# Optimization experiments

Measured on AMD Instinct MI355X. Metric: run time of the kernel, lower is better.

Reference implementation:

```python
import jax, jax.numpy as jnp
import numpy as np

B, T, D_IN, D_OUT = 4, 2048, 1024, 1024


def setup_inputs() -> dict:
    key = jax.random.key(0)
    k1, k2, k3, k4 = jax.random.split(key, 4)
    s = 0.02  # keep activations in a sane range
    x = jax.random.normal(k1, (B, T, D_IN), dtype=jnp.float32)
    Wq = jax.random.normal(k2, (D_IN, D_OUT), dtype=jnp.float32) * s
    Wk = jax.random.normal(k3, (D_IN, D_OUT), dtype=jnp.float32) * s
    Wv = jax.random.normal(k4, (D_IN, D_OUT), dtype=jnp.float32) * s
    return {"x": x, "Wq": Wq, "Wk": Wk, "Wv": Wv}


def reference(x, Wq, Wk, Wv):
    # Linear projections (torch Linear: y = x @ W^T, here W stored as [d_in, d_out])
    q = jnp.einsum('btd,de->bte', x, Wq)
    k = jnp.einsum('btd,de,->bte', x, Wk, jnp.float32(1.0)) if False else jnp.einsum('btd,de->bte', x, Wk)
    v = jnp.einsum('btd,de->bte', x, Wv)
    # Full [B, T, T] score matrix (faithful to the hand-rolled implementation)
    scores = jnp.einsum('bqe,bke->bqk', q, k)
    T_ = x.shape[1]
    causal = jnp.triu(jnp.ones((T_, T_), dtype=bool), k=1)  # True above diagonal
    scores = jnp.where(causal[None, :, :], -jnp.inf, scores)
    scale = 1.0 / jnp.sqrt(jnp.asarray(k.shape[-1], dtype=scores.dtype))
    attn = jax.nn.softmax(scores * scale, axis=-1)
    # dropout p=0.0 -> identity
    return jnp.einsum('bqk,bke->bqe', attn, v)
```

## Files before the change

### kernel.cpp

```cpp
#include <hip/hip_runtime.h>
#include <hip/hip_bf16.h>
#include <cstdint>

typedef __attribute__((ext_vector_type(8))) short short8;
typedef __attribute__((ext_vector_type(4))) float floatx4;

__device__ __forceinline__ float bf2f(unsigned short u) {
  unsigned int x = ((unsigned int)u) << 16;
  return __builtin_bit_cast(float, x);
}
__device__ __forceinline__ unsigned short f2bf(float f) {
  unsigned int x = __builtin_bit_cast(unsigned int, f);
  x += 0x7fffu + ((x >> 16) & 1u);
  return (unsigned short)(x >> 16);
}

__device__ __forceinline__ void gload_lds16(const void* g, void* l) {
  __builtin_amdgcn_global_load_lds(
      (const __attribute__((address_space(1))) void*)g,
      (__attribute__((address_space(3))) void*)l, 16, 0, 0);
}


__global__ __launch_bounds__(256) void cvtx_kernel(const float* __restrict__ x,
                                                   unsigned short* __restrict__ xb) {
  int i = blockIdx.x * 256 + threadIdx.x;
  const float4* xf = (const float4*)x;
  float4 a = xf[i * 2], b = xf[i * 2 + 1];
  short8 o;
  o[0] = (short)f2bf(a.x); o[1] = (short)f2bf(a.y);
  o[2] = (short)f2bf(a.z); o[3] = (short)f2bf(a.w);
  o[4] = (short)f2bf(b.x); o[5] = (short)f2bf(b.y);
  o[6] = (short)f2bf(b.z); o[7] = (short)f2bf(b.w);
  ((short8*)xb)[i] = o;
}

__global__ __launch_bounds__(256) void wt_kernel(const float* __restrict__ Wq,
                                                 const float* __restrict__ Wk,
                                                 const float* __restrict__ Wv,
                                                 unsigned short* __restrict__ Wt) {
  int z = blockIdx.z;
  const float* W = z == 0 ? Wq : (z == 1 ? Wk : Wv);
  unsigned short* O = Wt + (size_t)z * 1024 * 1024;
  __shared__ float tile[64][65];
  int c0 = blockIdx.x * 64;
  int r0 = blockIdx.y * 64;
  int tid = threadIdx.x;
#pragma unroll
  for (int i = 0; i < 4; ++i) {
    int c = tid + i * 256; int rr = c >> 4, q = c & 15;
    float4 v = *(const float4*)&W[(size_t)(r0 + rr) * 1024 + c0 + q * 4];
    tile[rr][q * 4 + 0] = v.x; tile[rr][q * 4 + 1] = v.y;
    tile[rr][q * 4 + 2] = v.z; tile[rr][q * 4 + 3] = v.w;
  }
  __syncthreads();
#pragma unroll
  for (int i = 0; i < 2; ++i) {
    int c = tid + i * 256; int oc = c >> 3, q = c & 7;
    short8 o;
#pragma unroll
    for (int j = 0; j < 8; ++j) o[j] = (short)f2bf(tile[q * 8 + j][oc]);
    *(short8*)&O[(size_t)(c0 + oc) * 1024 + r0 + q * 8] = o;
  }
}

__global__ __launch_bounds__(256) void vt_kernel(const unsigned short* __restrict__ V,
                                                 unsigned short* __restrict__ Vt) {
  int b = blockIdx.z;
  const unsigned short* Vb = V + (size_t)b * 2048 * 1024;
  unsigned short* Vtb = Vt + (size_t)b * 1024 * 2048;
  __shared__ unsigned short tile[64][72];
  int t0 = blockIdx.x * 64;
  int e0 = blockIdx.y * 64;
  int tid = threadIdx.x;
#pragma unroll
  for (int i = 0; i < 2; ++i) {
    int c = tid + i * 256; int rr = c >> 3, q = c & 7;
    short8 s = *(const short8*)&Vb[(size_t)(t0 + rr) * 1024 + e0 + q * 8];
#pragma unroll
    for (int j = 0; j < 8; ++j) tile[rr][q * 8 + j] = (unsigned short)s[j];
  }
  __syncthreads();
#pragma unroll
  for (int i = 0; i < 2; ++i) {
    int c = tid + i * 256; int er = c >> 3, q = c & 7;
    short8 o;
#pragma unroll
    for (int j = 0; j < 8; ++j) o[j] = (short)tile[q * 8 + j][er];
    *(short8*)&Vtb[(size_t)(e0 + er) * 2048 + t0 + q * 8] = o;
  }
}


template <bool OUT_BF16>
__device__ __forceinline__ void gemm_tn_core(const unsigned short* __restrict__ A,
                                             const unsigned short* __restrict__ B,
                                             void* __restrict__ C,
                                             int lda, int ldb, int ldc,
                                             int m0, int n0, int kTiles) {
  __shared__ __align__(16) unsigned short Asm[2][128 * 32];
  __shared__ __align__(16) unsigned short Bsm[2][128 * 32];
  const int tid = threadIdx.x;
  const int lane = tid & 63;
  const int wave = tid >> 6;
  const int wrow = (wave >> 1) * 64;
  const int wcol = (wave & 1) * 64;
  const int r15 = lane & 15;
  const int kg = (lane >> 4) * 8;

  floatx4 acc[4][4] = {};

  const unsigned short* Ag = A + (size_t)m0 * lda;
  const unsigned short* Bg = B + (size_t)n0 * ldb;

  auto stage = [&](int buf, int kt) {
    int k0 = kt * 32;
#pragma unroll
    for (int i = 0; i < 2; ++i) {
      int c = tid + i * 256;
      gload_lds16(Ag + (size_t)(c >> 2) * lda + k0 + (c & 3) * 8, &Asm[buf][c * 8]);
    }
#pragma unroll
    for (int i = 0; i < 2; ++i) {
      int c = tid + i * 256;
      gload_lds16(Bg + (size_t)(c >> 2) * ldb + k0 + (c & 3) * 8, &Bsm[buf][c * 8]);
    }
  };

  stage(0, 0);
  for (int kt = 0; kt < kTiles; ++kt) {
    int cur = kt & 1;
    __syncthreads();
    if (kt + 1 < kTiles) stage(cur ^ 1, kt + 1);
    const unsigned short* As = Asm[cur];
    const unsigned short* Bs = Bsm[cur];
    short8 af[4], bfr[4];
#pragma unroll
    for (int m = 0; m < 4; ++m)
      af[m] = *(const short8*)&As[(wrow + m * 16 + r15) * 32 + kg];
#pragma unroll
    for (int n = 0; n < 4; ++n)
      bfr[n] = *(const short8*)&Bs[(wcol + n * 16 + r15) * 32 + kg];
#pragma unroll
    for (int m = 0; m < 4; ++m)
#pragma unroll
      for (int n = 0; n < 4; ++n)
        acc[m][n] = __builtin_amdgcn_mfma_f32_16x16x32_bf16(af[m], bfr[n], acc[m][n], 0, 0, 0);
  }

  const int rq = (lane >> 4) * 4;
#pragma unroll
  for (int m = 0; m < 4; ++m) {
#pragma unroll
    for (int n = 0; n < 4; ++n) {
      int gc = n0 + wcol + n * 16 + r15;
#pragma unroll
      for (int r = 0; r < 4; ++r) {
        int gr = m0 + wrow + m * 16 + rq + r;
        if (OUT_BF16)
          ((unsigned short*)C)[(size_t)gr * ldc + gc] = f2bf(acc[m][n][r]);
        else
          ((float*)C)[(size_t)gr * ldc + gc] = acc[m][n][r];
      }
    }
  }
}

__global__ __launch_bounds__(256) void qkv_kernel(const unsigned short* __restrict__ Xb,
                                                  const unsigned short* __restrict__ Wt,
                                                  unsigned short* __restrict__ QKV) {
  gemm_tn_core<true>(Xb, Wt + (size_t)blockIdx.z * 1024 * 1024,
                     QKV + (size_t)blockIdx.z * 8192 * 1024,
                     1024, 1024, 1024, blockIdx.x * 128, blockIdx.y * 128, 32);
}

__global__ __launch_bounds__(256) void s_kernel(const unsigned short* __restrict__ Q,
                                                const unsigned short* __restrict__ K,
                                                unsigned short* __restrict__ S) {
  int t = blockIdx.x;
  int qb = (int)((sqrtf(8.f * (float)t + 1.f) - 1.f) * 0.5f);
  while ((qb + 1) * (qb + 2) / 2 <= t) ++qb;
  while (qb * (qb + 1) / 2 > t) --qb;
  int kb = t - qb * (qb + 1) / 2;
  size_t b = blockIdx.y;
  gemm_tn_core<true>(Q + b * 2048 * 1024, K + b * 2048 * 1024, S + b * 2048 * 2048,
                     1024, 1024, 2048, qb * 128, kb * 128, 32);
}

__global__ __launch_bounds__(256) void pv_kernel(const unsigned short* __restrict__ P,
                                                 const unsigned short* __restrict__ Vt,
                                                 float* __restrict__ O) {
  int qb = blockIdx.x;
  size_t b = blockIdx.z;
  gemm_tn_core<false>(P + b * 2048 * 2048, Vt + b * 1024 * 2048, O + b * 2048 * 1024,
                      2048, 2048, 1024, qb * 128, blockIdx.y * 128, (qb + 1) * 4);
}

__global__ __launch_bounds__(256) void softmax_kernel(unsigned short* __restrict__ S) {
  const int r = blockIdx.x;
  const int b = blockIdx.y;
  unsigned short* row = S + ((size_t)b * 2048 + r) * 2048;
  const int len = r + 1;
  const int padEnd = ((r >> 7) + 1) << 7;
  const int tid = threadIdx.x;
  const int base = tid * 8;
  const float scale = 0.03125f;

  float v[8];
  float mymax = -1e30f;
  if (base < len) {
    short8 s = *(const short8*)(row + base);
#pragma unroll
    for (int j = 0; j < 8; ++j) {
      float f = (base + j < len) ? bf2f((unsigned short)s[j]) : -1e30f;
      v[j] = f;
      mymax = fmaxf(mymax, f);
    }
  } else {
#pragma unroll
    for (int j = 0; j < 8; ++j) v[j] = -1e30f;
  }

  __shared__ float redm[4], reds[4];
  const int wave = tid >> 6, lane = tid & 63;
#pragma unroll
  for (int off = 32; off > 0; off >>= 1) mymax = fmaxf(mymax, __shfl_xor(mymax, off, 64));
  if (lane == 0) redm[wave] = mymax;
  __syncthreads();
  float m = fmaxf(fmaxf(redm[0], redm[1]), fmaxf(redm[2], redm[3])) * scale;

  float p[8];
  float mysum = 0.f;
#pragma unroll
  for (int j = 0; j < 8; ++j) {
    float e = (base + j < len) ? __expf(v[j] * scale - m) : 0.f;
    p[j] = e;
    mysum += e;
  }
#pragma unroll
  for (int off = 32; off > 0; off >>= 1) mysum += __shfl_xor(mysum, off, 64);
  if (lane == 0) reds[wave] = mysum;
  __syncthreads();
  float inv = 1.f / (reds[0] + reds[1] + reds[2] + reds[3]);

  if (base < padEnd) {
    short8 o;
#pragma unroll
    for (int j = 0; j < 8; ++j) o[j] = (short)f2bf(p[j] * inv);
    *(short8*)(row + base) = o;
  }
}


extern "C" void kernel_launch(void* const* d_in, const int* in_sizes, int n_in,
                              void* d_out, int out_size, void* d_ws, size_t ws_size,
                              hipStream_t stream) {
  const float* x  = (const float*)d_in[0];
  const float* Wq = (const float*)d_in[1];
  const float* Wk = (const float*)d_in[2];
  const float* Wv = (const float*)d_in[3];
  float* out = (float*)d_out;

  unsigned short* Xb  = (unsigned short*)d_ws;
  unsigned short* Wt  = Xb + (size_t)8192 * 1024;
  unsigned short* QKV = Wt + (size_t)3 * 1024 * 1024;
  unsigned short* Vt  = QKV + (size_t)3 * 8192 * 1024;
  unsigned short* S   = Vt + (size_t)4 * 1024 * 2048;

  const unsigned short* Qp = QKV;
  const unsigned short* Kp = QKV + (size_t)8192 * 1024;
  const unsigned short* Vp = QKV + (size_t)2 * 8192 * 1024;

  hipLaunchKernelGGL(cvtx_kernel, dim3(4096), dim3(256), 0, stream, x, Xb);
  hipLaunchKernelGGL(wt_kernel, dim3(16, 16, 3), dim3(256), 0, stream, Wq, Wk, Wv, Wt);
  hipLaunchKernelGGL(qkv_kernel, dim3(64, 8, 3), dim3(256), 0, stream, Xb, Wt, QKV);
  hipLaunchKernelGGL(vt_kernel, dim3(32, 16, 4), dim3(256), 0, stream, Vp, Vt);
  hipLaunchKernelGGL(s_kernel, dim3(136, 4), dim3(256), 0, stream, Qp, Kp, S);
  hipLaunchKernelGGL(softmax_kernel, dim3(2048, 4), dim3(256), 0, stream, S);
  hipLaunchKernelGGL(pv_kernel, dim3(16, 8, 4), dim3(256), 0, stream, S, Vt, out);
}
```

Before: 194.1 us.

## Replace QKV projection GEMM with 256x256 8-wave pipelined swizzled kernel

Replaces the 128x128 four-wave QKV projection GEMM with an eight-wave kernel using 256x256 output tiles over the fused 3072-wide weight matrix. It adds XOR-swizzled LDS layouts to avoid bank conflicts, a deeper multi-stage global-to-LDS prefetch with explicit vmcnt waits and barriers, MFMA priority boosting, and workgroup index swizzling for L2 locality. The goal is more data reuse per tile and better overlap of loads with MFMA work in the largest GEMM. The larger accumulator footprint raises register pressure, and the hand-placed waitcnt and barrier logic is fragile.

```diff
diff --git a/kernel.cpp b/kernel.cpp
--- a/kernel.cpp
+++ b/kernel.cpp
@@ -4,15 +4,16 @@
 
 typedef __attribute__((ext_vector_type(8))) short short8;
 typedef __attribute__((ext_vector_type(4))) float floatx4;
-
-__device__ __forceinline__ float bf2f(unsigned short u) {
+typedef unsigned short ushort;
+
+__device__ __forceinline__ float bf2f(ushort u) {
   unsigned int x = ((unsigned int)u) << 16;
   return __builtin_bit_cast(float, x);
 }
-__device__ __forceinline__ unsigned short f2bf(float f) {
+__device__ __forceinline__ ushort f2bf(float f) {
   unsigned int x = __builtin_bit_cast(unsigned int, f);
   x += 0x7fffu + ((x >> 16) & 1u);
-  return (unsigned short)(x >> 16);
+  return (ushort)(x >> 16);
 }
 
 __device__ __forceinline__ void gload_lds16(const void* g, void* l) {
@@ -23,7 +24,7 @@
 
 
 __global__ __launch_bounds__(256) void cvtx_kernel(const float* __restrict__ x,
-                                                   unsigned short* __restrict__ xb) {
+                                                   ushort* __restrict__ xb) {
   int i = blockIdx.x * 256 + threadIdx.x;
   const float4* xf = (const float4*)x;
   float4 a = xf[i * 2], b = xf[i * 2 + 1];
@@ -38,10 +39,10 @@
 __global__ __launch_bounds__(256) void wt_kernel(const float* __restrict__ Wq,
                                                  const float* __restrict__ Wk,
                                                  const float* __restrict__ Wv,
-                                                 unsigned short* __restrict__ Wt) {
+                                                 ushort* __restrict__ Wt) {
   int z = blockIdx.z;
   const float* W = z == 0 ? Wq : (z == 1 ? Wk : Wv);
-  unsigned short* O = Wt + (size_t)z * 1024 * 1024;
+  ushort* O = Wt + (size_t)z * 1024 * 1024;
   __shared__ float tile[64][65];
   int c0 = blockIdx.x * 64;
   int r0 = blockIdx.y * 64;
@@ -64,12 +65,12 @@
   }
 }
 
-__global__ __launch_bounds__(256) void vt_kernel(const unsigned short* __restrict__ V,
-                                                 unsigned short* __restrict__ Vt) {
+__global__ __launch_bounds__(256) void vt_kernel(const ushort* __restrict__ V,
+                                                 ushort* __restrict__ Vt) {
   int b = blockIdx.z;
-  const unsigned short* Vb = V + (size_t)b * 2048 * 1024;
-  unsigned short* Vtb = Vt + (size_t)b * 1024 * 2048;
-  __shared__ unsigned short tile[64][72];
+  const ushort* Vb = V + (size_t)b * 2048 * 1024;
+  ushort* Vtb = Vt + (size_t)b * 1024 * 2048;
+  __shared__ ushort tile[64][72];
   int t0 = blockIdx.x * 64;
   int e0 = blockIdx.y * 64;
   int tid = threadIdx.x;
@@ -78,7 +79,7 @@
     int c = tid + i * 256; int rr = c >> 3, q = c & 7;
     short8 s = *(const short8*)&Vb[(size_t)(t0 + rr) * 1024 + e0 + q * 8];
 #pragma unroll
-    for (int j = 0; j < 8; ++j) tile[rr][q * 8 + j] = (unsigned short)s[j];
+    for (int j = 0; j < 8; ++j) tile[rr][q * 8 + j] = (ushort)s[j];
   }
   __syncthreads();
 #pragma unroll
@@ -92,14 +93,127 @@
 }
 
 
+__global__ __launch_bounds__(512, 2) void qkv8_kernel(const ushort* __restrict__ A,
+                                                      const ushort* __restrict__ Bm,
+                                                      ushort* __restrict__ QKV) {
+  __shared__ __align__(16) ushort lds[2][2][2][8192];
+
+  const int tid = threadIdx.x;
+  const int lane = tid & 63;
+  const int wave = tid >> 6;
+  const int wm = wave >> 2;
+  const int wn = wave & 3;
+  const int r15 = lane & 15;
+  const int kg = lane >> 4;
+
+  const int nwgx = 32, nwgy = 12;
+  int orig = blockIdx.y * nwgx + blockIdx.x;
+  int swz = (orig & 7) * ((nwgx * nwgy) >> 3) + (orig >> 3);
+  int by = swz % nwgy;
+  int bx = swz / nwgy;
+  const int m0 = bx * 256;
+  const int n0 = by * 256;
+
+  const ushort* Ag = A + (size_t)m0 * 1024;
+  const ushort* Bg = Bm + (size_t)n0 * 1024;
+
+  const int NKT = 16;
+
+  floatx4 acc[8][4] = {};
+
+  auto stage = [&](int sidx) {
+    int kt = sidx >> 2, hh = sidx & 3;
+    int mat = hh & 1, kh = hh >> 1;
+    ushort* dst = &lds[kt & 1][mat][kh][0];
+    const ushort* src = mat ? Bg : Ag;
+    int kbase = kt * 64 + kh * 32;
+#pragma unroll
+    for (int i = 0; i < 2; ++i) {
+      int t = tid + i * 512;
+      int d = t * 16;
+      int L = d ^ (((d >> 7) & 3) << 4);
+      int row = L >> 6;
+      int colE = (L & 63) >> 1;
+      gload_lds16(src + (size_t)row * 1024 + kbase + colE, dst + t * 8);
+    }
+  };
+
+  auto ldA = [&](int buf, int ks, int m) -> short8 {
+    int row = wm * 128 + m * 16 + r15;
+    int L = row * 64 + kg * 16;
+    int P = L ^ (((row >> 1) & 3) << 4);
+    return *(const short8*)((const char*)&lds[buf][0][ks][0] + P);
+  };
+  auto ldB = [&](int buf, int ks, int n) -> short8 {
+    int row = wn * 64 + n * 16 + r15;
+    int L = row * 64 + kg * 16;
+    int P = L ^ (((row >> 1) & 3) << 4);
+    return *(const short8*)((const char*)&lds[buf][1][ks][0] + P);
+  };
+
+  for (int s = 0; s < 6; ++s) stage(s);
+  asm volatile("s_waitcnt vmcnt(8)" ::: "memory");
+  __builtin_amdgcn_s_barrier();
+
+  short8 bfrag[4];
+  int sidx = 6;
+  for (int kt = 0; kt < NKT; ++kt) {
+    int cur = kt & 1;
+#pragma unroll
+    for (int q = 0; q < 4; ++q) {
+      const int ks = q >> 1;
+      const int msub = (q & 1) * 4;
+      short8 afrag[4];
+      if ((q & 1) == 0) {
+#pragma unroll
+        for (int n = 0; n < 4; ++n) bfrag[n] = ldB(cur, ks, n);
+      }
+#pragma unroll
+      for (int m = 0; m < 4; ++m) afrag[m] = ldA(cur, ks, msub + m);
+      if (sidx < NKT * 4) stage(sidx);
+      ++sidx;
+      if (q & 1) asm volatile("s_waitcnt vmcnt(4)" ::: "memory");
+      __builtin_amdgcn_s_barrier();
+      asm volatile("s_waitcnt lgkmcnt(0)" ::: "memory");
+      __builtin_amdgcn_sched_barrier(0);
+      __builtin_amdgcn_s_setprio(1);
+#pragma unroll
+      for (int m = 0; m < 4; ++m)
+#pragma unroll
+        for (int n = 0; n < 4; ++n)
+          acc[msub + m][n] =
+              __builtin_amdgcn_mfma_f32_16x16x32_bf16(afrag[m], bfrag[n], acc[msub + m][n], 0, 0, 0);
+      __builtin_amdgcn_s_setprio(0);
+      __builtin_amdgcn_s_barrier();
+    }
+  }
+
+  ushort* Cz = QKV + (size_t)(n0 >> 10) * 8192 * 1024;
+  const int cb = n0 & 1023;
+  const int rq = kg * 4;
+#pragma unroll
+  for (int m = 0; m < 8; ++m) {
+#pragma unroll
+    for (int n = 0; n < 4; ++n) {
+      int gc = cb + wn * 64 + n * 16 + r15;
+#pragma unroll
+      for (int r = 0; r < 4; ++r) {
+        int gr = m0 + wm * 128 + m * 16 + rq + r;
+        Cz[(size_t)gr * 1024 + gc] = f2bf(acc[m][n][r]);
+      }
+    }
+  }
+}
+
+
 template <bool OUT_BF16>
-__device__ __forceinline__ void gemm_tn_core(const unsigned short* __restrict__ A,
-                                             const unsigned short* __restrict__ B,
+__device__ __forceinline__ void gemm_tn_core(const ushort* __restrict__ A,
+                                             const ushort* __restrict__ B,
                                              void* __restrict__ C,
                                              int lda, int ldb, int ldc,
                                              int m0, int n0, int kTiles) {
-  __shared__ __align__(16) unsigned short Asm[2][128 * 32];
-  __shared__ __align__(16) unsigned short Bsm[2][128 * 32];
+  __shared__ __align__(16) ushort Asm[2][128 * 32];
+  __shared__ __align__(16) ushort Bsm[2][128 * 32];
   const int tid = threadIdx.x;
   const int lane = tid & 63;
   const int wave = tid >> 6;
@@ -110,8 +224,8 @@
 
   floatx4 acc[4][4] = {};
 
-  const unsigned short* Ag = A + (size_t)m0 * lda;
-  const unsigned short* Bg = B + (size_t)n0 * ldb;
+  const ushort* Ag = A + (size_t)m0 * lda;
+  const ushort* Bg = B + (size_t)n0 * ldb;
 
   auto stage = [&](int buf, int kt) {
     int k0 = kt * 32;
@@ -132,8 +246,8 @@
     int cur = kt & 1;
     __syncthreads();
     if (kt + 1 < kTiles) stage(cur ^ 1, kt + 1);
-    const unsigned short* As = Asm[cur];
-    const unsigned short* Bs = Bsm[cur];
+    const ushort* As = Asm[cur];
+    const ushort* Bs = Bsm[cur];
     short8 af[4], bfr[4];
 #pragma unroll
     for (int m = 0; m < 4; ++m)
@@ -158,7 +272,7 @@
       for (int r = 0; r < 4; ++r) {
         int gr = m0 + wrow + m * 16 + rq + r;
         if (OUT_BF16)
-          ((unsigned short*)C)[(size_t)gr * ldc + gc] = f2bf(acc[m][n][r]);
+          ((ushort*)C)[(size_t)gr * ldc + gc] = f2bf(acc[m][n][r]);
         else
           ((float*)C)[(size_t)gr * ldc + gc] = acc[m][n][r];
       }
@@ -166,17 +280,9 @@
   }
 }
 
-__global__ __launch_bounds__(256) void qkv_kernel(const unsigned short* __restrict__ Xb,
-                                                  const unsigned short* __restrict__ Wt,
-                                                  unsigned short* __restrict__ QKV) {
-  gemm_tn_core<true>(Xb, Wt + (size_t)blockIdx.z * 1024 * 1024,
-                     QKV + (size_t)blockIdx.z * 8192 * 1024,
-                     1024, 1024, 1024, blockIdx.x * 128, blockIdx.y * 128, 32);
-}
-
-__global__ __launch_bounds__(256) void s_kernel(const unsigned short* __restrict__ Q,
-                                                const unsigned short* __restrict__ K,
-                                                unsigned short* __restrict__ S) {
+__global__ __launch_bounds__(256) void s_kernel(const ushort* __restrict__ Q,
+                                                const ushort* __restrict__ K,
+                                                ushort* __restrict__ S) {
   int t = blockIdx.x;
   int qb = (int)((sqrtf(8.f * (float)t + 1.f) - 1.f) * 0.5f);
   while ((qb + 1) * (qb + 2) / 2 <= t) ++qb;
@@ -187,8 +293,8 @@
                      1024, 1024, 2048, qb * 128, kb * 128, 32);
 }
 
-__global__ __launch_bounds__(256) void pv_kernel(const unsigned short* __restrict__ P,
-                                                 const unsigned short* __restrict__ Vt,
+__global__ __launch_bounds__(256) void pv_kernel(const ushort* __restrict__ P,
+                                                 const ushort* __restrict__ Vt,
                                                  float* __restrict__ O) {
   int qb = blockIdx.x;
   size_t b = blockIdx.z;
@@ -196,10 +302,10 @@
                       2048, 2048, 1024, qb * 128, blockIdx.y * 128, (qb + 1) * 4);
 }
 
-__global__ __launch_bounds__(256) void softmax_kernel(unsigned short* __restrict__ S) {
+__global__ __launch_bounds__(256) void softmax_kernel(ushort* __restrict__ S) {
   const int r = blockIdx.x;
   const int b = blockIdx.y;
-  unsigned short* row = S + ((size_t)b * 2048 + r) * 2048;
+  ushort* row = S + ((size_t)b * 2048 + r) * 2048;
   const int len = r + 1;
   const int padEnd = ((r >> 7) + 1) << 7;
   const int tid = threadIdx.x;
@@ -212,7 +318,7 @@
     short8 s = *(const short8*)(row + base);
 #pragma unroll
     for (int j = 0; j < 8; ++j) {
-      float f = (base + j < len) ? bf2f((unsigned short)s[j]) : -1e30f;
+      float f = (base + j < len) ? bf2f((ushort)s[j]) : -1e30f;
       v[j] = f;
       mymax = fmaxf(mymax, f);
     }
@@ -261,19 +367,19 @@
   const float* Wv = (const float*)d_in[3];
   float* out = (float*)d_out;
 
-  unsigned short* Xb  = (unsigned short*)d_ws;
-  unsigned short* Wt  = Xb + (size_t)8192 * 1024;
-  unsigned short* QKV = Wt + (size_t)3 * 1024 * 1024;
-  unsigned short* Vt  = QKV + (size_t)3 * 8192 * 1024;
-  unsigned short* S   = Vt + (size_t)4 * 1024 * 2048;
-
-  const unsigned short* Qp = QKV;
-  const unsigned short* Kp = QKV + (size_t)8192 * 1024;
-  const unsigned short* Vp = QKV + (size_t)2 * 8192 * 1024;
+  ushort* Xb  = (ushort*)d_ws;
+  ushort* Wt  = Xb + (size_t)8192 * 1024;
+  ushort* QKV = Wt + (size_t)3 * 1024 * 1024;
+  ushort* Vt  = QKV + (size_t)3 * 8192 * 1024;
+  ushort* S   = Vt + (size_t)4 * 1024 * 2048;
+
+  const ushort* Qp = QKV;
+  const ushort* Kp = QKV + (size_t)8192 * 1024;
+  const ushort* Vp = QKV + (size_t)2 * 8192 * 1024;
 
   hipLaunchKernelGGL(cvtx_kernel, dim3(4096), dim3(256), 0, stream, x, Xb);
   hipLaunchKernelGGL(wt_kernel, dim3(16, 16, 3), dim3(256), 0, stream, Wq, Wk, Wv, Wt);
-  hipLaunchKernelGGL(qkv_kernel, dim3(64, 8, 3), dim3(256), 0, stream, Xb, Wt, QKV);
+  hipLaunchKernelGGL(qkv8_kernel, dim3(32, 12), dim3(512), 0, stream, Xb, Wt, QKV);
   hipLaunchKernelGGL(vt_kernel, dim3(32, 16, 4), dim3(256), 0, stream, Vp, Vt);
   hipLaunchKernelGGL(s_kernel, dim3(136, 4), dim3(256), 0, stream, Qp, Kp, S);
   hipLaunchKernelGGL(softmax_kernel, dim3(2048, 4), dim3(256), 0, stream, S);
```

After: 188.7 us. 2.8% less time.
